# Optimization experiments

Hardware: AMD Instinct MI355X
Metric: run time of the kernel (lower is better)

Reference implementation:

```python
import jax, jax.numpy as jnp
import numpy as np

TEMPS = (0.02, 0.05, 0.2)
EPS = 1e-06


def _pairwise_dist_sq(x, y):
    # (N, M) squared L2 distances, clamped at 0 like the torch version
    dsq = (x * x).sum(-1)[:, None] + (y * y).sum(-1)[None, :] - 2.0 * (x @ y.T)
    return jnp.maximum(dsq, 0.0)


def reference(gen_features, pos_features, drift_scales):
    gen, pos = gen_features, pos_features
    N = gen.shape[0]
    # Distances are temperature-independent; compute once and reuse across temps.
    d_att = jnp.sqrt(_pairwise_dist_sq(gen, pos))  # (N_gen, N_pos)
    eye = jnp.eye(N, dtype=bool)
    dsq_rep = _pairwise_dist_sq(gen, gen)
    # diagonal gets masked to -inf in the logits anyway; replace 0 before sqrt for numerical safety
    d_rep = jnp.sqrt(jnp.where(eye, 1.0, dsq_rep))  # (N_gen, N_gen)

    drift_sum = jnp.zeros_like(gen)
    for i, T in enumerate(TEMPS):
        # attraction: sum_j softmax(-d/T)_ij * (pos_j - gen_i) == softmax @ pos - gen
        # (weights sum to 1 along axis=1, so the -gen_i term factors out)
        w_att = jax.nn.softmax(-d_att / T, axis=1)
        attraction = w_att @ pos - gen
        # repulsion: self-pair excluded via -inf logit (masked_fill(inf) on distances)
        logits_rep = jnp.where(eye, -jnp.inf, -d_rep / T)
        w_rep = jax.nn.softmax(logits_rep, axis=1)
        repulsion = w_rep @ gen - gen
        scale = jnp.maximum(drift_scales[i], EPS)
        drift_sum = drift_sum + (attraction - repulsion) / scale
    return drift_sum / len(TEMPS)


def setup_inputs() -> dict:
    key = jax.random.key(0)
    k1, k2 = jax.random.split(key)
    return {
        "gen_features": jax.random.normal(k1, (8192, 1024), dtype=jnp.float32),
        "pos_features": jax.random.normal(k2, (8192, 1024), dtype=jnp.float32),
        "drift_scales": jnp.ones((3,), dtype=jnp.float32),
    }
```

## Files before the change

kernel.cpp:

```cpp
#include <hip/hip_runtime.h>
#include <hip/hip_bf16.h>

#define NN 8192
#define DD 1024
#define KK 16384

using half8 = __attribute__((ext_vector_type(8))) _Float16;
using half4 = __attribute__((ext_vector_type(4))) _Float16;
using f32x4 = __attribute__((ext_vector_type(4))) float;
using u32x4 = __attribute__((ext_vector_type(4))) unsigned int;

__device__ __align__(16) _Float16 g_gh[(size_t)NN * DD];
__device__ __align__(16) _Float16 g_ph[(size_t)NN * DD];
__device__ __align__(16) _Float16 g_vt[(size_t)DD * KK];
__device__ float g_gn[NN];
__device__ float g_pn[NN];
__device__ __align__(16) unsigned short g_datt[(size_t)NN * NN];
__device__ __align__(16) unsigned short g_drep[(size_t)NN * NN];
__device__ __align__(16) _Float16 g_w[(size_t)NN * KK];
__device__ float g_part[2 * (size_t)NN * DD];

typedef const __attribute__((address_space(1))) void GV;
typedef __attribute__((address_space(3))) void LV;
__device__ inline void gload16(const void* g, void* l) {
    __builtin_amdgcn_global_load_lds((GV*)g, (LV*)l, 16, 0, 0);
}

__global__ __launch_bounds__(256) void k_conv(const float* __restrict__ gen,
                                              const float* __restrict__ pos) {
    int b = blockIdx.x;
    int r = b & (NN - 1);
    const float* src = (b < NN) ? gen : pos;
    _Float16* dsth = (b < NN) ? g_gh : g_ph;
    float* dstn = (b < NN) ? g_gn : g_pn;
    int t = threadIdx.x;
    const float4* s4 = (const float4*)(src + (size_t)r * DD);
    float4 x = s4[t];
    half4 h = {(_Float16)x.x, (_Float16)x.y, (_Float16)x.z, (_Float16)x.w};
    *(half4*)(dsth + (size_t)r * DD + t * 4) = h;
    float s = x.x * x.x + x.y * x.y + x.z * x.z + x.w * x.w;
#pragma unroll
    for (int off = 32; off; off >>= 1) s += __shfl_xor(s, off);
    __shared__ float red[4];
    if ((t & 63) == 0) red[t >> 6] = s;
    __syncthreads();
    if (t == 0) dstn[r] = red[0] + red[1] + red[2] + red[3];
}

__global__ __launch_bounds__(256) void k_tr(const float* __restrict__ pos,
                                            const float* __restrict__ gen) {
    int jt = blockIdx.x;
    int dt = blockIdx.y;
    int z = blockIdx.z;
    const float* src = z ? gen : pos;
    size_t cbase = z ? (size_t)NN : 0;
    __shared__ _Float16 tile[64][68];
    int t = threadIdx.x;
    int j0 = jt * 64, d0 = dt * 64;
#pragma unroll
    for (int p = 0; p < 4; p++) {
        int idx = t + p * 256;
        int r = idx >> 4;
        int c4 = idx & 15;
        float4 x = *(const float4*)(src + (size_t)(j0 + r) * DD + d0 + c4 * 4);
        tile[r][c4 * 4 + 0] = (_Float16)x.x;
        tile[r][c4 * 4 + 1] = (_Float16)x.y;
        tile[r][c4 * 4 + 2] = (_Float16)x.z;
        tile[r][c4 * 4 + 3] = (_Float16)x.w;
    }
    __syncthreads();
#pragma unroll
    for (int p = 0; p < 4; p++) {
        int idx = t + p * 256;
        int d = idx >> 4;
        int j4 = idx & 15;
        half4 h = {tile[j4 * 4 + 0][d], tile[j4 * 4 + 1][d],
                   tile[j4 * 4 + 2][d], tile[j4 * 4 + 3][d]};
        *(half4*)(g_vt + (size_t)(d0 + d) * KK + cbase + j0 + j4 * 4) = h;
    }
}

#define MFMA16(A_, B_, C_) __builtin_amdgcn_mfma_f32_16x16x32_f16(A_, B_, C_, 0, 0, 0)
#define BAR() __builtin_amdgcn_s_barrier()
#define LGKM0() do { asm volatile("s_waitcnt lgkmcnt(0)" ::: "memory"); \
                     __builtin_amdgcn_sched_barrier(0); } while (0)
#define VM4() asm volatile("s_waitcnt vmcnt(4)" ::: "memory")
#define VM0() asm volatile("s_waitcnt vmcnt(0)" ::: "memory")

template <int LDK>
__device__ inline void gemm_core(const _Float16* __restrict__ A,
                                 const _Float16* __restrict__ B,
                                 int arow0, int brow0, int kcol0, int ntiles,
                                 _Float16* lds, f32x4 acc[8][4]) {
    int t = threadIdx.x;
    int w = t >> 6, lane = t & 63;
    int wm = w >> 2, wn = w & 3;
    int q = lane >> 4, li = lane & 15;
    _Float16* sA = lds;
    _Float16* sB = lds + 4 * 8192;

    int offA[8], offB[4];
#pragma unroll
    for (int m = 0; m < 8; ++m) {
        int row = wm * 128 + m * 16 + li;
        offA[m] = row * 32 + (q ^ ((row >> 1) & 3)) * 8;
    }
#pragma unroll
    for (int n = 0; n < 4; ++n) {
        int row = wn * 64 + n * 16 + li;
        offB[n] = row * 32 + (q ^ ((row >> 1) & 3)) * 8;
    }

    int rbase = w * 16 + (lane >> 2);
    int csrc = (lane & 3) ^ ((rbase >> 1) & 3);
    const _Float16* gA0 = A + (size_t)(arow0 + rbase) * LDK + kcol0 + csrc * 8;
    const _Float16* gA1 = gA0 + (size_t)128 * LDK;
    const _Float16* gB0 = B + (size_t)(brow0 + rbase) * LDK + kcol0 + csrc * 8;
    const _Float16* gB1 = gB0 + (size_t)128 * LDK;
    int ldst = w * 512;

#define STAGE_A(tile_) do { \
    gload16(gA0 + (size_t)(tile_) * 32, sA + ((tile_) & 3) * 8192 + ldst); \
    gload16(gA1 + (size_t)(tile_) * 32, sA + ((tile_) & 3) * 8192 + 4096 + ldst); } while (0)
#define STAGE_B(tile_) do { \
    gload16(gB0 + (size_t)(tile_) * 32, sB + ((tile_) & 3) * 8192 + ldst); \
    gload16(gB1 + (size_t)(tile_) * 32, sB + ((tile_) & 3) * 8192 + 4096 + ldst); } while (0)

    STAGE_A(0); STAGE_B(0); STAGE_A(1); STAGE_B(1);
    VM4();
    BAR();

    int nwin = ntiles >> 1;
    half8 af[4], bf[4], af2[4];
#pragma unroll 2
    for (int wi = 0; wi < nwin; ++wi) {
        int t0 = 2 * wi, t1 = t0 + 1;
        const _Float16* a0 = sA + (t0 & 3) * 8192;
        const _Float16* b0 = sB + (t0 & 3) * 8192;
        const _Float16* a1 = sA + (t1 & 3) * 8192;
        const _Float16* b1 = sB + (t1 & 3) * 8192;
#pragma unroll
        for (int m = 0; m < 4; ++m) af[m] = *(const half8*)(a0 + offA[m]);
#pragma unroll
        for (int n = 0; n < 4; ++n) bf[n] = *(const half8*)(b0 + offB[n]);
        if (t0 + 2 < ntiles) STAGE_A(t0 + 2);
        BAR();
        LGKM0();
        __builtin_amdgcn_s_setprio(1);
#pragma unroll
        for (int m = 0; m < 4; ++m)
#pragma unroll
            for (int n = 0; n < 4; ++n)
                acc[m][n] = MFMA16(af[m], bf[n], acc[m][n]);
        __builtin_amdgcn_s_setprio(0);
        BAR();
#pragma unroll
        for (int m = 0; m < 4; ++m) af2[m] = *(const half8*)(a0 + offA[m + 4]);
        if (t0 + 2 < ntiles) STAGE_B(t0 + 2);
        BAR();
        LGKM0();
        __builtin_amdgcn_s_setprio(1);
#pragma unroll
        for (int m = 0; m < 4; ++m)
#pragma unroll
            for (int n = 0; n < 4; ++n)
                acc[m + 4][n] = MFMA16(af2[m], bf[n], acc[m + 4][n]);
        __builtin_amdgcn_s_setprio(0);
        if (wi < nwin - 1) VM4(); else VM0();
        BAR();
#pragma unroll
        for (int m = 0; m < 4; ++m) af[m] = *(const half8*)(a1 + offA[m]);
#pragma unroll
        for (int n = 0; n < 4; ++n) bf[n] = *(const half8*)(b1 + offB[n]);
        if (t1 + 2 < ntiles) STAGE_A(t1 + 2);
        BAR();
        LGKM0();
        __builtin_amdgcn_s_setprio(1);
#pragma unroll
        for (int m = 0; m < 4; ++m)
#pragma unroll
            for (int n = 0; n < 4; ++n)
                acc[m][n] = MFMA16(af[m], bf[n], acc[m][n]);
        __builtin_amdgcn_s_setprio(0);
        BAR();
#pragma unroll
        for (int m = 0; m < 4; ++m) af2[m] = *(const half8*)(a1 + offA[m + 4]);
        if (t1 + 2 < ntiles) STAGE_B(t1 + 2);
        BAR();
        LGKM0();
        __builtin_amdgcn_s_setprio(1);
#pragma unroll
        for (int m = 0; m < 4; ++m)
#pragma unroll
            for (int n = 0; n < 4; ++n)
                acc[m + 4][n] = MFMA16(af2[m], bf[n], acc[m + 4][n]);
        __builtin_amdgcn_s_setprio(0);
        if (wi < nwin - 1) {
            VM4();
            BAR();
        }
    }
#undef STAGE_A
#undef STAGE_B
}

__global__ __launch_bounds__(512, 2) void k_qk2() {
    extern __shared__ _Float16 lds[];
    int id = blockIdx.y * 32 + blockIdx.x;
    id = (id & 7) * 128 + (id >> 3);
    int rt = id >> 5, ct = id & 31;
    int rep = blockIdx.z;
    const _Float16* A = g_gh;
    const _Float16* B = rep ? g_gh : g_ph;
    const float* An = g_gn;
    const float* Bn = rep ? g_gn : g_pn;
    unsigned short* outp = rep ? g_drep : g_datt;

    f32x4 acc[8][4] = {};
    gemm_core<DD>(A, B, rt * 256, ct * 256, 0, DD / 32, lds, acc);
    __syncthreads();

    int t = threadIdx.x, w = t >> 6, lane = t & 63;
    int wm = w >> 2, wn = w & 3, q = lane >> 4, li = lane & 15;
    unsigned short* sd = (unsigned short*)lds;
    float bnv[4];
#pragma unroll
    for (int n = 0; n < 4; ++n) bnv[n] = Bn[ct * 256 + wn * 64 + n * 16 + li];
#pragma unroll
    for (int m = 0; m < 8; ++m) {
        int row0 = wm * 128 + m * 16 + q * 4;
#pragma unroll
        for (int r = 0; r < 4; ++r) {
            int row = row0 + r;
            float an = An[rt * 256 + row];
#pragma unroll
            for (int n = 0; n < 4; ++n) {
                int col = wn * 64 + n * 16 + li;
                float dsq = an + bnv[n] - 2.0f * acc[m][n][r];
                float d = sqrtf(fmaxf(dsq, 0.0f));
                if (rep && (rt * 256 + row) == (ct * 256 + col)) d = 1e30f;
                float dv = fminf(d * 1024.0f + 0.5f, 65535.0f);
                sd[row * 256 + col] = (unsigned short)(int)dv;
            }
        }
    }
    __syncthreads();
    const u32x4* s4 = (const u32x4*)sd;
    int row16 = t >> 5, chunk = t & 31;
#pragma unroll
    for (int i = 0; i < 16; ++i) {
        int lrow = i * 16 + row16;
        u32x4 v = s4[lrow * 32 + chunk];
        u32x4* gp = (u32x4*)(outp + (size_t)(rt * 256 + lrow) * NN + ct * 256) + chunk;
        __builtin_nontemporal_store(v, gp);
    }
}

__global__ __launch_bounds__(256) void k_sw(const float* __restrict__ scales) {
    int i = blockIdx.x, t = threadIdx.x;
    const u32x4* ra = (const u32x4*)(g_datt + (size_t)i * NN);
    const u32x4* rr = (const u32x4*)(g_drep + (size_t)i * NN);
    float va[32], vr[32];
    float mna = 1e30f, mnr = 1e30f;
    const float SC = 1.0f / 1024.0f;
#pragma unroll
    for (int p = 0; p < 4; ++p) {
        u32x4 x = __builtin_nontemporal_load(&ra[t + p * 256]);
        u32x4 y = __builtin_nontemporal_load(&rr[t + p * 256]);
#pragma unroll
        for (int u = 0; u < 4; ++u) {
            float a0 = (float)(x[u] & 0xFFFFu) * SC;
            float a1 = (float)(x[u] >> 16) * SC;
            float r0 = (float)(y[u] & 0xFFFFu) * SC;
            float r1 = (float)(y[u] >> 16) * SC;
            va[p * 8 + u * 2 + 0] = a0; va[p * 8 + u * 2 + 1] = a1;
            vr[p * 8 + u * 2 + 0] = r0; vr[p * 8 + u * 2 + 1] = r1;
            mna = fminf(mna, fminf(a0, a1));
            mnr = fminf(mnr, fminf(r0, r1));
        }
    }
#pragma unroll
    for (int off = 32; off; off >>= 1) {
        mna = fminf(mna, __shfl_xor(mna, off));
        mnr = fminf(mnr, __shfl_xor(mnr, off));
    }
    __shared__ float sm[2][4];
    __shared__ float ss[6][4];
    int wv = t >> 6;
    if ((t & 63) == 0) { sm[0][wv] = mna; sm[1][wv] = mnr; }
    __syncthreads();
    mna = fminf(fminf(sm[0][0], sm[0][1]), fminf(sm[0][2], sm[0][3]));
    mnr = fminf(fminf(sm[1][0], sm[1][1]), fminf(sm[1][2], sm[1][3]));
    float s0 = 0.f, s1 = 0.f, s2 = 0.f, s3 = 0.f, s4 = 0.f, s5 = 0.f;
#pragma unroll
    for (int k = 0; k < 32; ++k) {
        float da = va[k] - mna;
        s0 += __expf(da * -50.0f); s1 += __expf(da * -20.0f); s2 += __expf(da * -5.0f);
        float dr = vr[k] - mnr;
        s3 += __expf(dr * -50.0f); s4 += __expf(dr * -20.0f); s5 += __expf(dr * -5.0f);
    }
#pragma unroll
    for (int off = 32; off; off >>= 1) {
        s0 += __shfl_xor(s0, off); s1 += __shfl_xor(s1, off); s2 += __shfl_xor(s2, off);
        s3 += __shfl_xor(s3, off); s4 += __shfl_xor(s4, off); s5 += __shfl_xor(s5, off);
    }
    if ((t & 63) == 0) {
        ss[0][wv] = s0; ss[1][wv] = s1; ss[2][wv] = s2;
        ss[3][wv] = s3; ss[4][wv] = s4; ss[5][wv] = s5;
    }
    __syncthreads();
    float l0 = ss[0][0] + ss[0][1] + ss[0][2] + ss[0][3];
    float l1 = ss[1][0] + ss[1][1] + ss[1][2] + ss[1][3];
    float l2 = ss[2][0] + ss[2][1] + ss[2][2] + ss[2][3];
    float l3 = ss[3][0] + ss[3][1] + ss[3][2] + ss[3][3];
    float l4 = ss[4][0] + ss[4][1] + ss[4][2] + ss[4][3];
    float l5 = ss[5][0] + ss[5][1] + ss[5][2] + ss[5][3];
    float i0 = 1.0f / (3.0f * fmaxf(scales[0], 1e-6f));
    float i1 = 1.0f / (3.0f * fmaxf(scales[1], 1e-6f));
    float i2 = 1.0f / (3.0f * fmaxf(scales[2], 1e-6f));
    float ca0 = i0 / l0, ca1 = i1 / l1, ca2 = i2 / l2;
    float cr0 = -i0 / l3, cr1 = -i1 / l4, cr2 = -i2 / l5;
    _Float16* wa = g_w + (size_t)i * KK;
    _Float16* wr = wa + NN;
#pragma unroll
    for (int p = 0; p < 4; ++p) {
        union { half8 h; u32x4 u; } ha, hr;
#pragma unroll
        for (int qq = 0; qq < 8; ++qq) {
            float da = va[p * 8 + qq] - mna;
            ha.h[qq] = (_Float16)(ca0 * __expf(da * -50.0f) + ca1 * __expf(da * -20.0f) +
                                  ca2 * __expf(da * -5.0f));
            float dr = vr[p * 8 + qq] - mnr;
            hr.h[qq] = (_Float16)(cr0 * __expf(dr * -50.0f) + cr1 * __expf(dr * -20.0f) +
                                  cr2 * __expf(dr * -5.0f));
        }
        __builtin_nontemporal_store(ha.u, (u32x4*)(wa + (size_t)(t + p * 256) * 8));
        __builtin_nontemporal_store(hr.u, (u32x4*)(wr + (size_t)(t + p * 256) * 8));
    }
}

__global__ __launch_bounds__(512, 2) void k_gemm2() {
    extern __shared__ _Float16 lds[];
    int id = blockIdx.y * 4 + blockIdx.x;
    id = (id & 7) * 16 + (id >> 3);
    int rt = id >> 2, ct = id & 3;
    int z = blockIdx.z;
    f32x4 acc[8][4] = {};
    gemm_core<KK>(g_w, g_vt, rt * 256, ct * 256, z * (KK / 2), (KK / 2) / 32, lds, acc);
    float* outp = g_part + (size_t)z * NN * DD;
    int t = threadIdx.x, w = t >> 6, lane = t & 63;
    int wm = w >> 2, wn = w & 3, q = lane >> 4, li = lane & 15;
#pragma unroll
    for (int m = 0; m < 8; ++m) {
#pragma unroll
        for (int r = 0; r < 4; ++r) {
            int gi = rt * 256 + wm * 128 + m * 16 + q * 4 + r;
            float* orow = outp + (size_t)gi * DD;
#pragma unroll
            for (int n = 0; n < 4; ++n) {
                int gj = ct * 256 + wn * 64 + n * 16 + li;
                orow[gj] = acc[m][n][r];
            }
        }
    }
}

__global__ __launch_bounds__(256) void k_red(float* __restrict__ out) {
    size_t base = (size_t)blockIdx.x * 256 + threadIdx.x;
    const float4* p0 = (const float4*)g_part;
    const float4* p1 = (const float4*)(g_part + (size_t)NN * DD);
    float4* o4 = (float4*)out;
#pragma unroll
    for (int p = 0; p < 4; ++p) {
        size_t idx = base + (size_t)p * 524288;
        float4 a = p0[idx], b = p1[idx];
        float4 c = {a.x + b.x, a.y + b.y, a.z + b.z, a.w + b.w};
        o4[idx] = c;
    }
}

extern "C" void kernel_launch(void* const* d_in, const int* in_sizes, int n_in,
                              void* d_out, int out_size, void* d_ws, size_t ws_size,
                              hipStream_t stream) {
    (void)in_sizes; (void)n_in; (void)d_ws; (void)ws_size; (void)out_size;
    const float* gen = (const float*)d_in[0];
    const float* pos = (const float*)d_in[1];
    const float* scales = (const float*)d_in[2];

    (void)hipFuncSetAttribute((const void*)k_qk2, hipFuncAttributeMaxDynamicSharedMemorySize, 131072);
    (void)hipFuncSetAttribute((const void*)k_gemm2, hipFuncAttributeMaxDynamicSharedMemorySize, 131072);

    k_conv<<<dim3(2 * NN), 256, 0, stream>>>(gen, pos);
    k_tr<<<dim3(128, 16, 2), 256, 0, stream>>>(pos, gen);
    k_qk2<<<dim3(32, 32, 2), 512, 131072, stream>>>();
    k_sw<<<dim3(NN), 256, 0, stream>>>(scales);
    k_gemm2<<<dim3(4, 32, 2), 512, 131072, stream>>>();
    k_red<<<dim3(2048), 256, 0, stream>>>((float*)d_out);
}
```

Baseline: 832.2 us.

## Replace distance GEMM with smaller-tile single-buffered kernel for higher occupancy

```diff
diff --git a/kernel.cpp b/kernel.cpp
--- a/kernel.cpp
+++ b/kernel.cpp
@@ -87,6 +87,100 @@
 #define VM4() asm volatile("s_waitcnt vmcnt(4)" ::: "memory")
 #define VM0() asm volatile("s_waitcnt vmcnt(0)" ::: "memory")
 
+__global__ __launch_bounds__(256, 3) void k_qk3() {
+    __shared__ _Float16 sA[128 * 64];
+    __shared__ _Float16 sB[128 * 64];
+    int id = blockIdx.y * 64 + blockIdx.x;
+    id = (id & 7) * 512 + (id >> 3);
+    int rt = id >> 6, ct = id & 63;
+    int rep = blockIdx.z;
+    const _Float16* A = g_gh;
+    const _Float16* B = rep ? g_gh : g_ph;
+    const float* An = g_gn;
+    const float* Bn = rep ? g_gn : g_pn;
+    unsigned short* outp = rep ? g_drep : g_datt;
+
+    int t = threadIdx.x;
+    int w = t >> 6, lane = t & 63;
+    int wm = w >> 1, wn = w & 1;
+    int q = lane >> 4, li = lane & 15;
+
+    int offA_[4][2], offB_[4][2];
+#pragma unroll
+    for (int m = 0; m < 4; ++m) {
+        int rowa = wm * 64 + m * 16 + li;
+        int rowb = wn * 64 + m * 16 + li;
+#pragma unroll
+        for (int kk = 0; kk < 2; ++kk) {
+            offA_[m][kk] = rowa * 64 + ((kk * 4 + q) ^ (rowa & 7)) * 8;
+            offB_[m][kk] = rowb * 64 + ((kk * 4 + q) ^ (rowb & 7)) * 8;
+        }
+    }
+
+    int srow = t >> 3, sc = t & 7;
+    int csrc = sc ^ (srow & 7);
+    const _Float16* gA = A + (size_t)(rt * 128 + srow) * DD + csrc * 8;
+    const _Float16* gB = B + (size_t)(ct * 128 + srow) * DD + csrc * 8;
+    _Float16* dA = sA + t * 8;
+    _Float16* dB = sB + t * 8;
+
+    f32x4 acc[4][4] = {};
+    for (int kt = 0; kt < DD / 64; ++kt) {
+#pragma unroll
+        for (int r = 0; r < 4; ++r) {
+            gload16(gA + (size_t)(r * 32) * DD + kt * 64, dA + r * 2048);
+            gload16(gB + (size_t)(r * 32) * DD + kt * 64, dB + r * 2048);
+        }
+        __syncthreads();
+#pragma unroll
+        for (int kk = 0; kk < 2; ++kk) {
+            half8 a[4], b[4];
+#pragma unroll
+            for (int m = 0; m < 4; ++m) a[m] = *(const half8*)(sA + offA_[m][kk]);
+#pragma unroll
+            for (int n = 0; n < 4; ++n) b[n] = *(const half8*)(sB + offB_[n][kk]);
+#pragma unroll
+            for (int m = 0; m < 4; ++m)
+#pragma unroll
+                for (int n = 0; n < 4; ++n)
+                    acc[m][n] = MFMA16(a[m], b[n], acc[m][n]);
+        }
+        __syncthreads();
+    }
+
+    unsigned short* sd = (unsigned short*)sA;
+    float bnv[4];
+#pragma unroll
+    for (int n = 0; n < 4; ++n) bnv[n] = Bn[ct * 128 + wn * 64 + n * 16 + li];
+#pragma unroll
+    for (int m = 0; m < 4; ++m) {
+#pragma unroll
+        for (int r = 0; r < 4; ++r) {
+            int row = wm * 64 + m * 16 + q * 4 + r;
+            float an = An[rt * 128 + row];
+#pragma unroll
+            for (int n = 0; n < 4; ++n) {
+                int col = wn * 64 + n * 16 + li;
+                float dsq = an + bnv[n] - 2.0f * acc[m][n][r];
+                float d = sqrtf(fmaxf(dsq, 0.0f));
+                if (rep && (rt * 128 + row) == (ct * 128 + col)) d = 1e30f;
+                float dv = fminf(d * 1024.0f + 0.5f, 65535.0f);
+                sd[row * 128 + col] = (unsigned short)(int)dv;
+            }
+        }
+    }
+    __syncthreads();
+    const u32x4* s4 = (const u32x4*)sd;
+    int row16 = t >> 4, chunk = t & 15;
+#pragma unroll
+    for (int i = 0; i < 8; ++i) {
+        int lrow = i * 16 + row16;
+        u32x4 v = s4[lrow * 16 + chunk];
+        u32x4* gp = (u32x4*)(outp + (size_t)(rt * 128 + lrow) * NN + ct * 128) + chunk;
+        __builtin_nontemporal_store(v, gp);
+    }
+}
+
 template <int LDK>
 __device__ inline void gemm_core(const _Float16* __restrict__ A,
                                  const _Float16* __restrict__ B,
@@ -202,58 +296,6 @@
     }
 #undef STAGE_A
 #undef STAGE_B
-}
-
-__global__ __launch_bounds__(512, 2) void k_qk2() {
-    extern __shared__ _Float16 lds[];
-    int id = blockIdx.y * 32 + blockIdx.x;
-    id = (id & 7) * 128 + (id >> 3);
-    int rt = id >> 5, ct = id & 31;
-    int rep = blockIdx.z;
-    const _Float16* A = g_gh;
-    const _Float16* B = rep ? g_gh : g_ph;
-    const float* An = g_gn;
-    const float* Bn = rep ? g_gn : g_pn;
-    unsigned short* outp = rep ? g_drep : g_datt;
-
-    f32x4 acc[8][4] = {};
-    gemm_core<DD>(A, B, rt * 256, ct * 256, 0, DD / 32, lds, acc);
-    __syncthreads();
-
-    int t = threadIdx.x, w = t >> 6, lane = t & 63;
-    int wm = w >> 2, wn = w & 3, q = lane >> 4, li = lane & 15;
-    unsigned short* sd = (unsigned short*)lds;
-    float bnv[4];
-#pragma unroll
-    for (int n = 0; n < 4; ++n) bnv[n] = Bn[ct * 256 + wn * 64 + n * 16 + li];
-#pragma unroll
-    for (int m = 0; m < 8; ++m) {
-        int row0 = wm * 128 + m * 16 + q * 4;
-#pragma unroll
-        for (int r = 0; r < 4; ++r) {
-            int row = row0 + r;
-            float an = An[rt * 256 + row];
-#pragma unroll
-            for (int n = 0; n < 4; ++n) {
-                int col = wn * 64 + n * 16 + li;
-                float dsq = an + bnv[n] - 2.0f * acc[m][n][r];
-                float d = sqrtf(fmaxf(dsq, 0.0f));
-                if (rep && (rt * 256 + row) == (ct * 256 + col)) d = 1e30f;
-                float dv = fminf(d * 1024.0f + 0.5f, 65535.0f);
-                sd[row * 256 + col] = (unsigned short)(int)dv;
-            }
-        }
-    }
-    __syncthreads();
-    const u32x4* s4 = (const u32x4*)sd;
-    int row16 = t >> 5, chunk = t & 31;
-#pragma unroll
-    for (int i = 0; i < 16; ++i) {
-        int lrow = i * 16 + row16;
-        u32x4 v = s4[lrow * 32 + chunk];
-        u32x4* gp = (u32x4*)(outp + (size_t)(rt * 256 + lrow) * NN + ct * 256) + chunk;
-        __builtin_nontemporal_store(v, gp);
-    }
 }
 
 __global__ __launch_bounds__(256) void k_sw(const float* __restrict__ scales) {
@@ -387,12 +429,11 @@
     const float* pos = (const float*)d_in[1];
     const float* scales = (const float*)d_in[2];
 
-    (void)hipFuncSetAttribute((const void*)k_qk2, hipFuncAttributeMaxDynamicSharedMemorySize, 131072);
     (void)hipFuncSetAttribute((const void*)k_gemm2, hipFuncAttributeMaxDynamicSharedMemorySize, 131072);
 
     k_conv<<<dim3(2 * NN), 256, 0, stream>>>(gen, pos);
     k_tr<<<dim3(128, 16, 2), 256, 0, stream>>>(pos, gen);
-    k_qk2<<<dim3(32, 32, 2), 512, 131072, stream>>>();
+    k_qk3<<<dim3(64, 64, 2), 256, 0, stream>>>();
     k_sw<<<dim3(NN), 256, 0, stream>>>(scales);
     k_gemm2<<<dim3(4, 32, 2), 512, 131072, stream>>>();
     k_red<<<dim3(2048), 256, 0, stream>>>((float*)d_out);
```

After: 913.6 us. 1.1x slower.

## Replace distance GEMM kernel with 256x128-tile, 4-wave, triple-buffered variant

Applied to the files above, without the earlier changes.

```diff
diff --git a/kernel.cpp b/kernel.cpp
--- a/kernel.cpp
+++ b/kernel.cpp
@@ -85,7 +85,118 @@
 #define LGKM0() do { asm volatile("s_waitcnt lgkmcnt(0)" ::: "memory"); \
                      __builtin_amdgcn_sched_barrier(0); } while (0)
 #define VM4() asm volatile("s_waitcnt vmcnt(4)" ::: "memory")
+#define VM6() asm volatile("s_waitcnt vmcnt(6)" ::: "memory")
 #define VM0() asm volatile("s_waitcnt vmcnt(0)" ::: "memory")
+
+__global__ __launch_bounds__(256, 2) void k_qk4() {
+    __shared__ _Float16 lds[3 * 12288];
+    int id = blockIdx.y * 64 + blockIdx.x;
+    id = (id & 7) * 256 + (id >> 3);
+    int rt = id >> 6, ct = id & 63;
+    int rep = blockIdx.z;
+    const _Float16* A = g_gh;
+    const _Float16* B = rep ? g_gh : g_ph;
+    const float* An = g_gn;
+    const float* Bn = rep ? g_gn : g_pn;
+    unsigned short* outp = rep ? g_drep : g_datt;
+
+    int t = threadIdx.x;
+    int w = t >> 6, lane = t & 63;
+    int wm = w >> 1, wn = w & 1;
+    int q = lane >> 4, li = lane & 15;
+
+    int offA[8], offB[4];
+#pragma unroll
+    for (int m = 0; m < 8; ++m) {
+        int row = wm * 128 + m * 16 + li;
+        offA[m] = row * 32 + ((q ^ ((row >> 1) & 3)) * 8);
+    }
+#pragma unroll
+    for (int n = 0; n < 4; ++n) {
+        int row = wn * 64 + n * 16 + li;
+        offB[n] = 8192 + row * 32 + ((q ^ ((row >> 1) & 3)) * 8);
+    }
+
+    int srow = t >> 2;
+    int csrc = (t & 3) ^ ((srow >> 1) & 3);
+    const _Float16* gA = A + (size_t)(rt * 256 + srow) * DD + csrc * 8;
+    const _Float16* gB = B + (size_t)(ct * 128 + srow) * DD + csrc * 8;
+
+#define STAGE(tile_) do { \
+    _Float16* s_ = lds + ((tile_) % 3) * 12288; \
+    const _Float16* a_ = gA + (size_t)(tile_) * 32; \
+    const _Float16* b_ = gB + (size_t)(tile_) * 32; \
+    gload16(a_, s_ + t * 8); \
+    gload16(a_ + (size_t)64 * DD, s_ + t * 8 + 2048); \
+    gload16(a_ + (size_t)128 * DD, s_ + t * 8 + 4096); \
+    gload16(a_ + (size_t)192 * DD, s_ + t * 8 + 6144); \
+    gload16(b_, s_ + 8192 + t * 8); \
+    gload16(b_ + (size_t)64 * DD, s_ + 8192 + t * 8 + 2048); } while (0)
+
+    const int nt = DD / 32;
+    f32x4 acc[8][4] = {};
+
+    STAGE(0); STAGE(1);
+    VM6();
+    BAR();
+
+    for (int kt = 0; kt < nt; ++kt) {
+        const _Float16* s = lds + (kt % 3) * 12288;
+        half8 af[8], bf[4];
+#pragma unroll
+        for (int m = 0; m < 8; ++m) af[m] = *(const half8*)(s + offA[m]);
+#pragma unroll
+        for (int n = 0; n < 4; ++n) bf[n] = *(const half8*)(s + offB[n]);
+        if (kt + 2 < nt) STAGE(kt + 2);
+        BAR();
+        LGKM0();
+        __builtin_amdgcn_s_setprio(1);
+#pragma unroll
+        for (int m = 0; m < 8; ++m)
+#pragma unroll
+            for (int n = 0; n < 4; ++n)
+                acc[m][n] = MFMA16(af[m], bf[n], acc[m][n]);
+        __builtin_amdgcn_s_setprio(0);
+        if (kt < nt - 1) {
+            if (kt + 2 < nt) VM6(); else VM0();
+            BAR();
+        }
+    }
+#undef STAGE
+
+    __syncthreads();
+    unsigned short* sd = (unsigned short*)lds;
+    float bnv[4];
+#pragma unroll
+    for (int n = 0; n < 4; ++n) bnv[n] = Bn[ct * 128 + wn * 64 + n * 16 + li];
+#pragma unroll
+    for (int m = 0; m < 8; ++m) {
+#pragma unroll
+        for (int r = 0; r < 4; ++r) {
+            int row = wm * 128 + m * 16 + q * 4 + r;
+            float an = An[rt * 256 + row];
+#pragma unroll
+            for (int n = 0; n < 4; ++n) {
+                int col = wn * 64 + n * 16 + li;
+                float dsq = an + bnv[n] - 2.0f * acc[m][n][r];
+                float d = sqrtf(fmaxf(dsq, 0.0f));
+                if (rep && (rt * 256 + row) == (ct * 128 + col)) d = 1e30f;
+                float dv = fminf(d * 1024.0f + 0.5f, 65535.0f);
+                sd[row * 128 + col] = (unsigned short)(int)dv;
+            }
+        }
+    }
+    __syncthreads();
+    const u32x4* s4 = (const u32x4*)sd;
+#pragma unroll
+    for (int i = 0; i < 16; ++i) {
+        int idx = i * 256 + t;
+        int row = idx >> 4, chunk = idx & 15;
+        u32x4 v = s4[row * 16 + chunk];
+        u32x4* gp = (u32x4*)(outp + (size_t)(rt * 256 + row) * NN + ct * 128) + chunk;
+        __builtin_nontemporal_store(v, gp);
+    }
+}
 
 template <int LDK>
 __device__ inline void gemm_core(const _Float16* __restrict__ A,
@@ -202,58 +313,6 @@
     }
 #undef STAGE_A
 #undef STAGE_B
-}
-
-__global__ __launch_bounds__(512, 2) void k_qk2() {
-    extern __shared__ _Float16 lds[];
-    int id = blockIdx.y * 32 + blockIdx.x;
-    id = (id & 7) * 128 + (id >> 3);
-    int rt = id >> 5, ct = id & 31;
-    int rep = blockIdx.z;
-    const _Float16* A = g_gh;
-    const _Float16* B = rep ? g_gh : g_ph;
-    const float* An = g_gn;
-    const float* Bn = rep ? g_gn : g_pn;
-    unsigned short* outp = rep ? g_drep : g_datt;
-
-    f32x4 acc[8][4] = {};
-    gemm_core<DD>(A, B, rt * 256, ct * 256, 0, DD / 32, lds, acc);
-    __syncthreads();
-
-    int t = threadIdx.x, w = t >> 6, lane = t & 63;
-    int wm = w >> 2, wn = w & 3, q = lane >> 4, li = lane & 15;
-    unsigned short* sd = (unsigned short*)lds;
-    float bnv[4];
-#pragma unroll
-    for (int n = 0; n < 4; ++n) bnv[n] = Bn[ct * 256 + wn * 64 + n * 16 + li];
-#pragma unroll
-    for (int m = 0; m < 8; ++m) {
-        int row0 = wm * 128 + m * 16 + q * 4;
-#pragma unroll
-        for (int r = 0; r < 4; ++r) {
-            int row = row0 + r;
-            float an = An[rt * 256 + row];
-#pragma unroll
-            for (int n = 0; n < 4; ++n) {
-                int col = wn * 64 + n * 16 + li;
-                float dsq = an + bnv[n] - 2.0f * acc[m][n][r];
-                float d = sqrtf(fmaxf(dsq, 0.0f));
-                if (rep && (rt * 256 + row) == (ct * 256 + col)) d = 1e30f;
-                float dv = fminf(d * 1024.0f + 0.5f, 65535.0f);
-                sd[row * 256 + col] = (unsigned short)(int)dv;
-            }
-        }
-    }
-    __syncthreads();
-    const u32x4* s4 = (const u32x4*)sd;
-    int row16 = t >> 5, chunk = t & 31;
-#pragma unroll
-    for (int i = 0; i < 16; ++i) {
-        int lrow = i * 16 + row16;
-        u32x4 v = s4[lrow * 32 + chunk];
-        u32x4* gp = (u32x4*)(outp + (size_t)(rt * 256 + lrow) * NN + ct * 256) + chunk;
-        __builtin_nontemporal_store(v, gp);
-    }
 }
 
 __global__ __launch_bounds__(256) void k_sw(const float* __restrict__ scales) {
@@ -387,12 +446,11 @@
     const float* pos = (const float*)d_in[1];
     const float* scales = (const float*)d_in[2];
 
-    (void)hipFuncSetAttribute((const void*)k_qk2, hipFuncAttributeMaxDynamicSharedMemorySize, 131072);
     (void)hipFuncSetAttribute((const void*)k_gemm2, hipFuncAttributeMaxDynamicSharedMemorySize, 131072);
 
     k_conv<<<dim3(2 * NN), 256, 0, stream>>>(gen, pos);
     k_tr<<<dim3(128, 16, 2), 256, 0, stream>>>(pos, gen);
-    k_qk2<<<dim3(32, 32, 2), 512, 131072, stream>>>();
+    k_qk4<<<dim3(64, 32, 2), 256, 0, stream>>>();
     k_sw<<<dim3(NN), 256, 0, stream>>>(scales);
     k_gemm2<<<dim3(4, 32, 2), 512, 131072, stream>>>();
     k_red<<<dim3(2048), 256, 0, stream>>>((float*)d_out);
```

Result: slower. 869.5 us (+4.5%).

## Exploit symmetry of gen-gen distance matrix by computing only lower-triangular tiles

Applied to the files above, without the earlier changes.

```diff
diff --git a/kernel.cpp b/kernel.cpp
--- a/kernel.cpp
+++ b/kernel.cpp
@@ -206,10 +206,19 @@
 
 __global__ __launch_bounds__(512, 2) void k_qk2() {
     extern __shared__ _Float16 lds[];
-    int id = blockIdx.y * 32 + blockIdx.x;
-    id = (id & 7) * 128 + (id >> 3);
-    int rt = id >> 5, ct = id & 31;
-    int rep = blockIdx.z;
+    int id = blockIdx.x;
+    id = (id & 7) * 194 + (id >> 3);
+    int rep, rt, ct;
+    if (id < 1024) {
+        rep = 0; rt = id >> 5; ct = id & 31;
+    } else {
+        rep = 1;
+        int k = id - 1024;
+        int r = (int)((sqrtf(8.0f * (float)k + 1.0f) - 1.0f) * 0.5f);
+        while ((r + 1) * (r + 2) / 2 <= k) ++r;
+        while (r * (r + 1) / 2 > k) --r;
+        rt = r; ct = k - r * (r + 1) / 2;
+    }
     const _Float16* A = g_gh;
     const _Float16* B = rep ? g_gh : g_ph;
     const float* An = g_gn;
@@ -226,17 +235,22 @@
     float bnv[4];
 #pragma unroll
     for (int n = 0; n < 4; ++n) bnv[n] = Bn[ct * 256 + wn * 64 + n * 16 + li];
+    float anv[8][4];
+#pragma unroll
+    for (int m = 0; m < 8; ++m)
+#pragma unroll
+        for (int r = 0; r < 4; ++r)
+            anv[m][r] = An[rt * 256 + wm * 128 + m * 16 + q * 4 + r];
+
 #pragma unroll
     for (int m = 0; m < 8; ++m) {
-        int row0 = wm * 128 + m * 16 + q * 4;
 #pragma unroll
         for (int r = 0; r < 4; ++r) {
-            int row = row0 + r;
-            float an = An[rt * 256 + row];
+            int row = wm * 128 + m * 16 + q * 4 + r;
 #pragma unroll
             for (int n = 0; n < 4; ++n) {
                 int col = wn * 64 + n * 16 + li;
-                float dsq = an + bnv[n] - 2.0f * acc[m][n][r];
+                float dsq = anv[m][r] + bnv[n] - 2.0f * acc[m][n][r];
                 float d = sqrtf(fmaxf(dsq, 0.0f));
                 if (rep && (rt * 256 + row) == (ct * 256 + col)) d = 1e30f;
                 float dv = fminf(d * 1024.0f + 0.5f, 65535.0f);
@@ -245,14 +259,45 @@
         }
     }
     __syncthreads();
-    const u32x4* s4 = (const u32x4*)sd;
-    int row16 = t >> 5, chunk = t & 31;
-#pragma unroll
-    for (int i = 0; i < 16; ++i) {
-        int lrow = i * 16 + row16;
-        u32x4 v = s4[lrow * 32 + chunk];
-        u32x4* gp = (u32x4*)(outp + (size_t)(rt * 256 + lrow) * NN + ct * 256) + chunk;
-        __builtin_nontemporal_store(v, gp);
+    {
+        const u32x4* s4 = (const u32x4*)sd;
+        int row16 = t >> 5, chunk = t & 31;
+#pragma unroll
+        for (int i = 0; i < 16; ++i) {
+            int lrow = i * 16 + row16;
+            u32x4 v = s4[lrow * 32 + chunk];
+            __builtin_nontemporal_store(
+                v, (u32x4*)(outp + (size_t)(rt * 256 + lrow) * NN + ct * 256) + chunk);
+        }
+    }
+
+    if (rep && rt != ct) {
+        __syncthreads();
+#pragma unroll
+        for (int m = 0; m < 8; ++m) {
+#pragma unroll
+            for (int r = 0; r < 4; ++r) {
+                int row = wm * 128 + m * 16 + q * 4 + r;
+#pragma unroll
+                for (int n = 0; n < 4; ++n) {
+                    int col = wn * 64 + n * 16 + li;
+                    float dsq = anv[m][r] + bnv[n] - 2.0f * acc[m][n][r];
+                    float d = sqrtf(fmaxf(dsq, 0.0f));
+                    float dv = fminf(d * 1024.0f + 0.5f, 65535.0f);
+                    sd[col * 256 + row] = (unsigned short)(int)dv;
+                }
+            }
+        }
+        __syncthreads();
+        const u32x4* s4 = (const u32x4*)sd;
+        int row16 = t >> 5, chunk = t & 31;
+#pragma unroll
+        for (int i = 0; i < 16; ++i) {
+            int lrow = i * 16 + row16;
+            u32x4 v = s4[lrow * 32 + chunk];
+            __builtin_nontemporal_store(
+                v, (u32x4*)(outp + (size_t)(ct * 256 + lrow) * NN + rt * 256) + chunk);
+        }
     }
 }
 
@@ -392,7 +437,7 @@
 
     k_conv<<<dim3(2 * NN), 256, 0, stream>>>(gen, pos);
     k_tr<<<dim3(128, 16, 2), 256, 0, stream>>>(pos, gen);
-    k_qk2<<<dim3(32, 32, 2), 512, 131072, stream>>>();
+    k_qk2<<<dim3(1552), 512, 131072, stream>>>();
     k_sw<<<dim3(NN), 256, 0, stream>>>(scales);
     k_gemm2<<<dim3(4, 32, 2), 512, 131072, stream>>>();
     k_red<<<dim3(2048), 256, 0, stream>>>((float*)d_out);
```

After: 809.0 us, median of 2. 2.8% less time.
